# Optimization experiments

Measured on AMD Instinct MI355X. Metric: run time of the kernel, lower is better.

Reference implementation:

```python
import jax, jax.numpy as jnp
import numpy as np

EPS = 1e-5  # torch GroupNorm default eps

def gn(x, g, b):
    # GroupNorm with 1 group on [..., C]: normalize over channel dim, per-channel affine
    m = jnp.mean(x, axis=-1, keepdims=True)
    v = jnp.var(x, axis=-1, keepdims=True)
    return (x - m) * jax.lax.rsqrt(v + EPS) * g + b

def linear_res(x, W1, g1, b1, W2, g2, b2):
    # LaneGCN LinearRes (n_in == n_out, identity shortcut)
    out = jax.nn.relu(gn(x @ W1, g1, b1))
    out = gn(out @ W2, g2, b2)
    return jax.nn.relu(out + x)

def setup_inputs() -> dict:
    key = jax.random.key(0)
    N, K, P, D = 100000, 6, 30, 128
    ks = jax.random.split(key, 12)
    s = 0.05
    f32 = jnp.float32
    return dict(
        actors=jax.random.normal(ks[0], (N, D), f32),
        actor_ctrs=jax.random.normal(ks[1], (N, 2), f32) * 50.0,
        pred_W1=jax.random.normal(ks[2], (K, D, D), f32) * s,
        pred_g1=jnp.ones((K, D), f32), pred_b1=jnp.zeros((K, D), f32),
        pred_W2=jax.random.normal(ks[3], (K, D, D), f32) * s,
        pred_g2=jnp.ones((K, D), f32), pred_b2=jnp.zeros((K, D), f32),
        pred_Wo=jax.random.normal(ks[4], (K, D, 2 * P), f32) * s,
        pred_bo=jnp.zeros((K, 2 * P), f32),
        dist_W0=jax.random.normal(ks[5], (2, D), f32) * s,
        dist_b0=jnp.zeros((D,), f32),
        dist_W1=jax.random.normal(ks[6], (D, D), f32) * s,
        dist_g1=jnp.ones((D,), f32), dist_b1=jnp.zeros((D,), f32),
        agt_W=jax.random.normal(ks[7], (2 * D, D), f32) * s,
        agt_g=jnp.ones((D,), f32), agt_b=jnp.zeros((D,), f32),
        cls_W1=jax.random.normal(ks[8], (D, D), f32) * s,
        cls_g1=jnp.ones((D,), f32), cls_b1=jnp.zeros((D,), f32),
        cls_W2=jax.random.normal(ks[9], (D, D), f32) * s,
        cls_g2=jnp.ones((D,), f32), cls_b2=jnp.zeros((D,), f32),
        cls_Wo=jax.random.normal(ks[10], (D, 1), f32) * s,
        cls_bo=jnp.zeros((1,), f32),
    )

def reference(actors, actor_ctrs,
              pred_W1, pred_g1, pred_b1, pred_W2, pred_g2, pred_b2, pred_Wo, pred_bo,
              dist_W0, dist_b0, dist_W1, dist_g1, dist_b1,
              agt_W, agt_g, agt_b,
              cls_W1, cls_g1, cls_b1, cls_W2, cls_g2, cls_b2, cls_Wo, cls_bo):
    N, D = actors.shape
    K = pred_W1.shape[0]
    # --- num_mods prediction heads (LinearRes + Linear), vectorized over K ---
    h = jnp.einsum('nd,kde->kne', actors, pred_W1)
    h = jax.nn.relu(gn(h, pred_g1[:, None, :], pred_b1[:, None, :]))
    h = gn(jnp.einsum('kne,kef->knf', h, pred_W2), pred_g2[:, None, :], pred_b2[:, None, :])
    h = jax.nn.relu(h + actors[None])
    preds = jnp.einsum('knd,kdo->kno', h, pred_Wo) + pred_bo[:, None, :]   # [K,N,2P]
    reg = jnp.transpose(preds, (1, 0, 2)).reshape(N, K, -1, 2)             # [N,K,P,2]
    reg = reg + actor_ctrs[:, None, None, :]
    dest_ctrs = jax.lax.stop_gradient(reg[:, :, -1, :])                     # [N,K,2] (detach)
    # --- destination attention (myAttDestNoMap), vectorized over K modes ---
    dist = actor_ctrs[:, None, :] - dest_ctrs                              # [N,K,2]
    dh = jax.nn.relu(dist @ dist_W0 + dist_b0)
    dh = jax.nn.relu(gn(dh @ dist_W1, dist_g1, dist_b1))
    cat = jnp.concatenate([dh, jnp.broadcast_to(actors[:, None, :], (N, K, D))], axis=-1)
    feats = jax.nn.relu(gn(cat @ agt_W, agt_g, agt_b)).reshape(N * K, D)   # [N*K, D]
    # --- classification head + mode sorting ---
    c = linear_res(feats, cls_W1, cls_g1, cls_b1, cls_W2, cls_g2, cls_b2)
    cls = (c @ cls_Wo + cls_bo).reshape(N, K)
    cls = jax.nn.softmax(cls, axis=1)
    sort_idcs = jnp.argsort(-cls, axis=1)
    cls_sorted = jnp.take_along_axis(cls, sort_idcs, axis=1)               # [N,K]
    reg_sorted = jnp.take_along_axis(reg, sort_idcs[:, :, None, None], axis=1)  # [N,K,P,2]
    return cls_sorted, reg_sorted, feats
```

## Files before the change

kernel.cpp:

```cpp
#include <hip/hip_runtime.h>

#define NTOT 100000
#define KMOD 6

typedef short bf16x8 __attribute__((ext_vector_type(8)));
typedef float f32x4  __attribute__((ext_vector_type(4)));
typedef unsigned short u16x8 __attribute__((ext_vector_type(8)));

#define G1   0
#define B1O  128
#define G2   256
#define B2O  384
#define W0A  512
#define W0B  640
#define B0O  768
#define DG1  896
#define DB1  1024
#define AGTG 1152
#define AGTB 1280
#define CG1  1408
#define CB1O 1536
#define CG2  1664
#define CB2O 1792
#define CWO  1920
#define PBO  2048

__device__ __forceinline__ unsigned short f2bf(float f){
  union { float f; unsigned u; } c; c.f = f;
  return (unsigned short)((c.u + 0x7FFFu + ((c.u >> 16) & 1u)) >> 16);
}
__device__ __forceinline__ float bf2f(unsigned short h){
  union { unsigned u; float f; } c; c.u = ((unsigned)h) << 16; return c.f;
}

__global__ void prep_w(const float* __restrict__ W1, const float* __restrict__ W2,
                       const float* __restrict__ Wo, const float* __restrict__ dW1,
                       const float* __restrict__ agW, const float* __restrict__ cW1,
                       const float* __restrict__ cW2, unsigned short* __restrict__ dst){
  int e = blockIdx.x * 256 + threadIdx.x;
  if (e >= 327680) return;
  const float* base; int m = 0, r, CB = 8, Dreal = 128, mstride = 16384;
  if (e < 98304)       { base = W1;  m = e / 16384; r = e % 16384; }
  else if (e < 196608) { int x = e - 98304;  base = W2; m = x / 16384; r = x % 16384; }
  else if (e < 245760) { int x = e - 196608; base = Wo; m = x / 8192;  r = x % 8192; CB = 4; Dreal = 60; mstride = 7680; }
  else if (e < 262144) { base = dW1; r = e - 245760; }
  else if (e < 294912) { base = agW; r = e - 262144; }
  else if (e < 311296) { base = cW1; r = e - 294912; }
  else                 { base = cW2; r = e - 311296; }
  int per = CB * 512;
  int ks = r / per, rr = r % per;
  int cb = rr >> 9, l = (rr >> 3) & 63, j = rr & 7;
  int d = ks * 32 + ((l >> 4) << 3) + j;
  int c = (cb << 4) + (l & 15);
  float v = (c < Dreal) ? base[(size_t)m * mstride + d * Dreal + c] : 0.f;
  dst[e] = f2bf(v);
}

template<int CBN>
__device__ __forceinline__ void gemm2(const char* __restrict__ wsrc,
                                      const unsigned short* __restrict__ Xin,
                                      unsigned short* __restrict__ Wc, f32x4* acc){
  const int t = threadIdx.x, lane = t & 63, w = t >> 6;
  constexpr int chunk_bytes = CBN * 2048;
  constexpr int iters = chunk_bytes / 16 / 256;
  #pragma unroll
  for (int c = 0; c < 2; ++c){
    __syncthreads();
    const uint4* src = (const uint4*)(wsrc + c * chunk_bytes);
    uint4* dstv = (uint4*)Wc;
    #pragma unroll
    for (int i = 0; i < iters; ++i) dstv[t + i * 256] = src[t + i * 256];
    __syncthreads();
    #pragma unroll
    for (int ksl = 0; ksl < 2; ++ksl){
      const int ks = c * 2 + ksl;
      bf16x8 a = *(const bf16x8*)(Xin + ((w * 4 + ks) * 64 + lane) * 8);
      const unsigned short* wb = Wc + (ksl * CBN * 64 + lane) * 8;
      #pragma unroll
      for (int cb = 0; cb < CBN; ++cb){
        bf16x8 b = *(const bf16x8*)(wb + cb * 512);
        acc[cb] = __builtin_amdgcn_mfma_f32_16x16x32_bf16(a, b, acc[cb], 0, 0, 0);
      }
    }
  }
}

__device__ __forceinline__ void row_stats8(const f32x4* acc, float* mean, float* rstd){
  #pragma unroll
  for (int i = 0; i < 4; ++i){
    float s = 0.f, qq = 0.f;
    #pragma unroll
    for (int cb = 0; cb < 8; ++cb){ float v = acc[cb][i]; s += v; qq += v * v; }
    #pragma unroll
    for (int m = 1; m < 16; m <<= 1){ s += __shfl_xor(s, m, 16); qq += __shfl_xor(qq, m, 16); }
    float mu = s * 0.0078125f;
    float var = qq * 0.0078125f - mu * mu;
    mean[i] = mu; rstd[i] = rsqrtf(var + 1e-5f);
  }
}

__device__ __forceinline__ void epi_gn(const f32x4* acc, const float* cst, int goff, int boff,
                                       const unsigned short* res, unsigned short* Xout,
                                       float* feats_out, int n0, int kk){
  const int t = threadIdx.x, lane = t & 63, w = t >> 6, q = lane >> 4, c0 = lane & 15;
  float mean[4], rstd[4];
  row_stats8(acc, mean, rstd);
  #pragma unroll
  for (int cb = 0; cb < 8; ++cb){
    int col = c0 + (cb << 4);
    float g = cst[goff + col], bb = cst[boff + col];
    int base = ((w * 4 + (col >> 5)) * 64 + ((col >> 3) & 3) * 16) * 8 + (col & 7);
    #pragma unroll
    for (int i = 0; i < 4; ++i){
      int r15 = (q << 2) + i;
      float v = (acc[cb][i] - mean[i]) * rstd[i] * g + bb;
      if (res) v += bf2f(res[base + r15 * 8]);
      v = fmaxf(v, 0.f);
      if (feats_out){
        int n = n0 + w * 16 + r15;
        if (n < NTOT) feats_out[(size_t)(n * KMOD + kk) * 128 + col] = v;
      }
      Xout[base + r15 * 8] = f2bf(v);
    }
  }
}

#define ZACC(a, n) { _Pragma("unroll") for (int z = 0; z < (n); ++z){ (a)[z][0]=0.f;(a)[z][1]=0.f;(a)[z][2]=0.f;(a)[z][3]=0.f; } }

__global__ __launch_bounds__(256, 2) void meg(
    const float* __restrict__ actors, const float* __restrict__ ctrs,
    const float* __restrict__ pg1, const float* __restrict__ pb1,
    const float* __restrict__ pg2, const float* __restrict__ pb2,
    const float* __restrict__ pbo, const float* __restrict__ dW0, const float* __restrict__ db0,
    const float* __restrict__ dg1, const float* __restrict__ db1v,
    const float* __restrict__ agg, const float* __restrict__ agb,
    const float* __restrict__ cg1v, const float* __restrict__ cb1v,
    const float* __restrict__ cg2v, const float* __restrict__ cb2v,
    const float* __restrict__ cWo, const float* __restrict__ cbo,
    const unsigned short* __restrict__ wprep, float* __restrict__ logits,
    float* __restrict__ out_reg, float* __restrict__ out_feats){

  __shared__ __align__(16) unsigned short A0[8192];
  __shared__ __align__(16) unsigned short X1[8192];
  __shared__ __align__(16) unsigned short X2[8192];
  __shared__ __align__(16) unsigned short Wc[8192];
  __shared__ float cst[2176];
  __shared__ float ctr_l[128];
  __shared__ float dist_l[128];

  const int t = threadIdx.x;
  const int kk = blockIdx.x % KMOD;
  const int tile = blockIdx.x / KMOD;
  const int n0 = tile * 64;
  const int valid = min(64, NTOT - n0);
  const float cbo_v = cbo[0];

  if (t < 128){
    cst[G1 + t]   = pg1[kk * 128 + t];
    cst[B1O + t]  = pb1[kk * 128 + t];
    cst[G2 + t]   = pg2[kk * 128 + t];
    cst[B2O + t]  = pb2[kk * 128 + t];
    cst[W0A + t]  = dW0[t];
    cst[W0B + t]  = dW0[128 + t];
    cst[B0O + t]  = db0[t];
    cst[DG1 + t]  = dg1[t];
    cst[DB1 + t]  = db1v[t];
    cst[AGTG + t] = agg[t];
    cst[AGTB + t] = agb[t];
    cst[CG1 + t]  = cg1v[t];
    cst[CB1O + t] = cb1v[t];
    cst[CG2 + t]  = cg2v[t];
    cst[CB2O + t] = cb2v[t];
    cst[CWO + t]  = cWo[t];
  } else if (t < 192){
    int i = t - 128;
    cst[PBO + i] = (i < 60) ? pbo[kk * 60 + i] : 0.f;
  } else {
    int row = t - 192;
    if (row < valid){
      ctr_l[row * 2]     = ctrs[(size_t)(n0 + row) * 2];
      ctr_l[row * 2 + 1] = ctrs[(size_t)(n0 + row) * 2 + 1];
    } else { ctr_l[row * 2] = 0.f; ctr_l[row * 2 + 1] = 0.f; }
  }

  #pragma unroll
  for (int ii = 0; ii < 8; ++ii){
    int e2 = t + ii * 256;
    int row = e2 >> 5, c4 = e2 & 31;
    float4 v = make_float4(0.f, 0.f, 0.f, 0.f);
    if (row < valid) v = *(const float4*)(actors + (size_t)(n0 + row) * 128 + c4 * 4);
    int colb = c4 * 4;
    int idx = (((row >> 4) * 4 + (colb >> 5)) * 64 + (row & 15) + (((colb >> 3) & 3) << 4)) * 8 + (colb & 7);
    A0[idx]     = f2bf(v.x); A0[idx + 1] = f2bf(v.y);
    A0[idx + 2] = f2bf(v.z); A0[idx + 3] = f2bf(v.w);
  }

  const char* wp = (const char*)wprep;
  const char* W1k  = wp + (size_t)kk * 32768;
  const char* W2k  = wp + 196608 + (size_t)kk * 32768;
  const char* Wok  = wp + 393216 + (size_t)kk * 16384;
  const char* dW1p = wp + 491520;
  const char* agtp = wp + 524288;
  const char* cW1p = wp + 589824;
  const char* cW2p = wp + 622592;

  const int lane = t & 63, w = t >> 6, q = lane >> 4, c0 = lane & 15;
  f32x4 acc[8];

  ZACC(acc, 8);
  gemm2<8>(W1k, A0, Wc, acc);
  epi_gn(acc, cst, G1, B1O, nullptr, X1, nullptr, n0, kk);

  ZACC(acc, 8);
  gemm2<8>(W2k, X1, Wc, acc);
  epi_gn(acc, cst, G2, B2O, A0, X2, nullptr, n0, kk);

  {
    f32x4 acc4[4]; ZACC(acc4, 4);
    gemm2<4>(Wok, X2, Wc, acc4);
    #pragma unroll
    for (int cb = 0; cb < 4; ++cb){
      int col = c0 + (cb << 4);
      float bo = cst[PBO + col];
      #pragma unroll
      for (int i = 0; i < 4; ++i){
        int row = w * 16 + (q << 2) + i;
        float v = acc4[cb][i] + bo;
        if (col == 58) dist_l[row * 2]     = -v;
        if (col == 59) dist_l[row * 2 + 1] = -v;
        int n = n0 + row;
        if (col < 60 && n < NTOT)
          out_reg[(size_t)(n * KMOD + kk) * 60 + col] = v + ctr_l[row * 2 + (col & 1)];
      }
    }
  }
  __syncthreads();

  {
    int r15 = lane & 15;
    int row = w * 16 + r15;
    float d0 = dist_l[row * 2], d1 = dist_l[row * 2 + 1];
    #pragma unroll
    for (int ks = 0; ks < 4; ++ks){
      int dbase = ks * 32 + ((lane >> 4) << 3);
      u16x8 pack;
      #pragma unroll
      for (int j = 0; j < 8; ++j){
        int d = dbase + j;
        float v = fmaxf(d0 * cst[W0A + d] + d1 * cst[W0B + d] + cst[B0O + d], 0.f);
        pack[j] = f2bf(v);
      }
      *(u16x8*)(X1 + ((w * 4 + ks) * 64 + lane) * 8) = pack;
    }
  }

  ZACC(acc, 8);
  gemm2<8>(dW1p, X1, Wc, acc);
  epi_gn(acc, cst, DG1, DB1, nullptr, X2, nullptr, n0, kk);

  ZACC(acc, 8);
  gemm2<8>(agtp, X2, Wc, acc);
  gemm2<8>(agtp + 32768, A0, Wc, acc);
  epi_gn(acc, cst, AGTG, AGTB, nullptr, X1, out_feats, n0, kk);

  ZACC(acc, 8);
  gemm2<8>(cW1p, X1, Wc, acc);
  epi_gn(acc, cst, CG1, CB1O, nullptr, X2, nullptr, n0, kk);

  ZACC(acc, 8);
  gemm2<8>(cW2p, X2, Wc, acc);
  {
    float mean[4], rstd[4];
    row_stats8(acc, mean, rstd);
    float part[4] = {0.f, 0.f, 0.f, 0.f};
    #pragma unroll
    for (int cb = 0; cb < 8; ++cb){
      int col = c0 + (cb << 4);
      float g = cst[CG2 + col], bb = cst[CB2O + col], wo = cst[CWO + col];
      int base = ((w * 4 + (col >> 5)) * 64 + ((col >> 3) & 3) * 16) * 8 + (col & 7);
      #pragma unroll
      for (int i = 0; i < 4; ++i){
        int r15 = (q << 2) + i;
        float v = (acc[cb][i] - mean[i]) * rstd[i] * g + bb;
        v += bf2f(X1[base + r15 * 8]);
        v = fmaxf(v, 0.f);
        part[i] += v * wo;
      }
    }
    #pragma unroll
    for (int i = 0; i < 4; ++i){
      #pragma unroll
      for (int m = 1; m < 16; m <<= 1) part[i] += __shfl_xor(part[i], m, 16);
    }
    if (c0 == 0){
      #pragma unroll
      for (int i = 0; i < 4; ++i){
        int n = n0 + w * 16 + (q << 2) + i;
        if (n < NTOT) logits[n * KMOD + kk] = part[i] + cbo_v;
      }
    }
  }
}

__global__ __launch_bounds__(256) void fin(const float* __restrict__ logits,
                                           float* __restrict__ out_cls,
                                           float* __restrict__ out_reg){
  const int wid = blockIdx.x * 4 + (threadIdx.x >> 6);
  const int lane = threadIdx.x & 63;
  if (wid >= NTOT) return;
  const int n = wid;
  float lg[6];
  #pragma unroll
  for (int k2 = 0; k2 < 6; ++k2) lg[k2] = logits[n * 6 + k2];
  float mx = lg[0];
  #pragma unroll
  for (int k2 = 1; k2 < 6; ++k2) mx = fmaxf(mx, lg[k2]);
  float ex[6]; float s = 0.f;
  #pragma unroll
  for (int k2 = 0; k2 < 6; ++k2){ ex[k2] = expf(lg[k2] - mx); s += ex[k2]; }
  float inv = 1.f / s;
  int rank[6];
  #pragma unroll
  for (int k2 = 0; k2 < 6; ++k2){
    int r = 0;
    #pragma unroll
    for (int j2 = 0; j2 < 6; ++j2) r += (lg[j2] > lg[k2]) || (lg[j2] == lg[k2] && j2 < k2);
    rank[k2] = r;
  }
  if (lane < 6){
    float pv = 0.f;
    #pragma unroll
    for (int k2 = 0; k2 < 6; ++k2) pv += (rank[k2] == lane) ? ex[k2] : 0.f;
    out_cls[n * 6 + lane] = pv * inv;
  }
  if (lane < 60){
    float v[6];
    #pragma unroll
    for (int k2 = 0; k2 < 6; ++k2) v[k2] = out_reg[(size_t)(n * 6 + k2) * 60 + lane];
    #pragma unroll
    for (int r2 = 0; r2 < 6; ++r2){
      float ov = 0.f;
      #pragma unroll
      for (int k2 = 0; k2 < 6; ++k2) ov += (rank[k2] == r2) ? v[k2] : 0.f;
      out_reg[(size_t)(n * 6 + r2) * 60 + lane] = ov;
    }
  }
}

extern "C" void kernel_launch(void* const* d_in, const int* in_sizes, int n_in,
                              void* d_out, int out_size, void* d_ws, size_t ws_size,
                              hipStream_t stream){
  const float* actors = (const float*)d_in[0];
  const float* ctrs   = (const float*)d_in[1];
  const float* pW1 = (const float*)d_in[2];
  const float* pg1 = (const float*)d_in[3];
  const float* pb1 = (const float*)d_in[4];
  const float* pW2 = (const float*)d_in[5];
  const float* pg2 = (const float*)d_in[6];
  const float* pb2 = (const float*)d_in[7];
  const float* pWo = (const float*)d_in[8];
  const float* pbo = (const float*)d_in[9];
  const float* dW0 = (const float*)d_in[10];
  const float* db0 = (const float*)d_in[11];
  const float* dW1 = (const float*)d_in[12];
  const float* dg1 = (const float*)d_in[13];
  const float* db1 = (const float*)d_in[14];
  const float* agW = (const float*)d_in[15];
  const float* agg = (const float*)d_in[16];
  const float* agb = (const float*)d_in[17];
  const float* cW1 = (const float*)d_in[18];
  const float* cg1 = (const float*)d_in[19];
  const float* cb1 = (const float*)d_in[20];
  const float* cW2 = (const float*)d_in[21];
  const float* cg2 = (const float*)d_in[22];
  const float* cb2 = (const float*)d_in[23];
  const float* cWo = (const float*)d_in[24];
  const float* cbo = (const float*)d_in[25];

  float* logits = (float*)d_ws;
  unsigned short* wprep = (unsigned short*)((char*)d_ws + 2400256);
  float* out = (float*)d_out;
  float* out_cls   = out;
  float* out_reg   = out + 600000;
  float* out_feats = out + 36600000;

  hipLaunchKernelGGL(prep_w, dim3(1280), dim3(256), 0, stream,
                     pW1, pW2, pWo, dW1, agW, cW1, cW2, wprep);
  hipLaunchKernelGGL(meg, dim3(((NTOT + 63) / 64) * KMOD), dim3(256), 0, stream,
                     actors, ctrs, pg1, pb1, pg2, pb2, pbo, dW0, db0, dg1, db1,
                     agg, agb, cg1, cb1, cg2, cb2, cWo, cbo, wprep, logits, out_reg, out_feats);
  hipLaunchKernelGGL(fin, dim3(NTOT / 4), dim3(256), 0, stream, logits, out_cls, out_reg);
}
```

Before: 1.068 ms.

## Double-buffer weight loads via global_load_lds and use nontemporal output stores

Replaces the synchronous register-staged copy of weight chunks into LDS with direct global-to-LDS loads, issued per k-step into two alternating buffers so the next slice loads while MFMAs run on the current one. Large output writes (feats, regression) become nontemporal stores so they do not pollute cache. The manual waitcnt and barrier handling adds more barriers per GEMM (one before and one after each k-step) and is fragile if the vmcnt counts are wrong.

Result: faster. 1.041 ms (-2.5%).

```diff
diff --git a/kernel.cpp b/kernel.cpp
--- a/kernel.cpp
+++ b/kernel.cpp
@@ -31,6 +31,12 @@
 }
 __device__ __forceinline__ float bf2f(unsigned short h){
   union { unsigned u; float f; } c; c.u = ((unsigned)h) << 16; return c.f;
+}
+
+__device__ __forceinline__ void gload16(const void* g, void* l){
+  __builtin_amdgcn_global_load_lds(
+      (const __attribute__((address_space(1))) unsigned int*)g,
+      (__attribute__((address_space(3))) unsigned int*)l, 16, 0, 0);
 }
 
 __global__ void prep_w(const float* __restrict__ W1, const float* __restrict__ W2,
@@ -61,27 +67,40 @@
                                       const unsigned short* __restrict__ Xin,
                                       unsigned short* __restrict__ Wc, f32x4* acc){
   const int t = threadIdx.x, lane = t & 63, w = t >> 6;
-  constexpr int chunk_bytes = CBN * 2048;
-  constexpr int iters = chunk_bytes / 16 / 256;
-  #pragma unroll
-  for (int c = 0; c < 2; ++c){
-    __syncthreads();
-    const uint4* src = (const uint4*)(wsrc + c * chunk_bytes);
-    uint4* dstv = (uint4*)Wc;
-    #pragma unroll
-    for (int i = 0; i < iters; ++i) dstv[t + i * 256] = src[t + i * 256];
-    __syncthreads();
-    #pragma unroll
-    for (int ksl = 0; ksl < 2; ++ksl){
-      const int ks = c * 2 + ksl;
-      bf16x8 a = *(const bf16x8*)(Xin + ((w * 4 + ks) * 64 + lane) * 8);
-      const unsigned short* wb = Wc + (ksl * CBN * 64 + lane) * 8;
-      #pragma unroll
-      for (int cb = 0; cb < CBN; ++cb){
-        bf16x8 b = *(const bf16x8*)(wb + cb * 512);
-        acc[cb] = __builtin_amdgcn_mfma_f32_16x16x32_bf16(a, b, acc[cb], 0, 0, 0);
-      }
-    }
+  constexpr int kbytes = CBN * 1024;
+  constexpr int nld = kbytes / 4096;
+  char* wlds = (char*)Wc;
+  asm volatile("s_waitcnt lgkmcnt(0)" ::: "memory");
+  __builtin_amdgcn_s_barrier();
+  asm volatile("" ::: "memory");
+  #pragma unroll
+  for (int i = 0; i < nld; ++i)
+    gload16(wsrc + (t + i * 256) * 16, wlds + (t + i * 256) * 16);
+  #pragma unroll
+  for (int k = 0; k < 4; ++k){
+    if (k < 3){
+      const char* src = wsrc + (k + 1) * kbytes;
+      char* dstp = wlds + ((k + 1) & 1) * kbytes;
+      #pragma unroll
+      for (int i = 0; i < nld; ++i)
+        gload16(src + (t + i * 256) * 16, dstp + (t + i * 256) * 16);
+      if constexpr (nld == 2) asm volatile("s_waitcnt vmcnt(2)" ::: "memory");
+      else                    asm volatile("s_waitcnt vmcnt(1)" ::: "memory");
+    } else {
+      asm volatile("s_waitcnt vmcnt(0)" ::: "memory");
+    }
+    __builtin_amdgcn_s_barrier();
+    asm volatile("" ::: "memory");
+    bf16x8 a = *(const bf16x8*)(Xin + ((w * 4 + k) * 64 + lane) * 8);
+    const unsigned short* wb = Wc + (k & 1) * CBN * 512 + lane * 8;
+    #pragma unroll
+    for (int cb = 0; cb < CBN; ++cb){
+      bf16x8 b = *(const bf16x8*)(wb + cb * 512);
+      acc[cb] = __builtin_amdgcn_mfma_f32_16x16x32_bf16(a, b, acc[cb], 0, 0, 0);
+    }
+    asm volatile("s_waitcnt lgkmcnt(0)" ::: "memory");
+    __builtin_amdgcn_s_barrier();
+    asm volatile("" ::: "memory");
   }
 }
 
@@ -118,7 +137,8 @@
       v = fmaxf(v, 0.f);
       if (feats_out){
         int n = n0 + w * 16 + r15;
-        if (n < NTOT) feats_out[(size_t)(n * KMOD + kk) * 128 + col] = v;
+        if (n < NTOT)
+          __builtin_nontemporal_store(v, &feats_out[(size_t)(n * KMOD + kk) * 128 + col]);
       }
       Xout[base + r15 * 8] = f2bf(v);
     }
@@ -230,7 +250,8 @@
         if (col == 59) dist_l[row * 2 + 1] = -v;
         int n = n0 + row;
         if (col < 60 && n < NTOT)
-          out_reg[(size_t)(n * KMOD + kk) * 60 + col] = v + ctr_l[row * 2 + (col & 1)];
+          __builtin_nontemporal_store(v + ctr_l[row * 2 + (col & 1)],
+                                      &out_reg[(size_t)(n * KMOD + kk) * 60 + col]);
       }
     }
   }
```

## Stream GEMM weights from global into registers, removing LDS staging and block barriers

Applied to the files above, without the earlier changes.

Weights are no longer cooperatively copied into a shared Wc buffer between __syncthreads. Each wave now reads its B fragments directly from global or L2 into registers with double buffering, and the A fragments are held in registers. Per-layer constants are read straight from global instead of being staged in shared memory. Activation loading is remapped so each wave writes only its own rows, which lets the block barrier be replaced with a wave-local waitcnt. This cuts LDS footprint and block-level syncs, which should raise occupancy, but each wave now fetches the full weight matrix itself, so global and L2 traffic goes up several-fold.

Result: faster. 985.1 us (-7.7%).

```diff
diff --git a/kernel.cpp b/kernel.cpp
--- a/kernel.cpp
+++ b/kernel.cpp
@@ -6,24 +6,7 @@
 typedef short bf16x8 __attribute__((ext_vector_type(8)));
 typedef float f32x4  __attribute__((ext_vector_type(4)));
 typedef unsigned short u16x8 __attribute__((ext_vector_type(8)));
-
-#define G1   0
-#define B1O  128
-#define G2   256
-#define B2O  384
-#define W0A  512
-#define W0B  640
-#define B0O  768
-#define DG1  896
-#define DB1  1024
-#define AGTG 1152
-#define AGTB 1280
-#define CG1  1408
-#define CB1O 1536
-#define CG2  1664
-#define CB2O 1792
-#define CWO  1920
-#define PBO  2048
+typedef unsigned short u16x4 __attribute__((ext_vector_type(4)));
 
 __device__ __forceinline__ unsigned short f2bf(float f){
   union { float f; unsigned u; } c; c.f = f;
@@ -57,30 +40,30 @@
 }
 
 template<int CBN>
-__device__ __forceinline__ void gemm2(const char* __restrict__ wsrc,
-                                      const unsigned short* __restrict__ Xin,
-                                      unsigned short* __restrict__ Wc, f32x4* acc){
+__device__ __forceinline__ void gemmR(const char* __restrict__ wsrc,
+                                      const unsigned short* __restrict__ Xin, f32x4* acc){
   const int t = threadIdx.x, lane = t & 63, w = t >> 6;
-  constexpr int chunk_bytes = CBN * 2048;
-  constexpr int iters = chunk_bytes / 16 / 256;
-  #pragma unroll
-  for (int c = 0; c < 2; ++c){
-    __syncthreads();
-    const uint4* src = (const uint4*)(wsrc + c * chunk_bytes);
-    uint4* dstv = (uint4*)Wc;
-    #pragma unroll
-    for (int i = 0; i < iters; ++i) dstv[t + i * 256] = src[t + i * 256];
-    __syncthreads();
-    #pragma unroll
-    for (int ksl = 0; ksl < 2; ++ksl){
-      const int ks = c * 2 + ksl;
-      bf16x8 a = *(const bf16x8*)(Xin + ((w * 4 + ks) * 64 + lane) * 8);
-      const unsigned short* wb = Wc + (ksl * CBN * 64 + lane) * 8;
-      #pragma unroll
-      for (int cb = 0; cb < CBN; ++cb){
-        bf16x8 b = *(const bf16x8*)(wb + cb * 512);
-        acc[cb] = __builtin_amdgcn_mfma_f32_16x16x32_bf16(a, b, acc[cb], 0, 0, 0);
-      }
+  bf16x8 a[4];
+  #pragma unroll
+  for (int ks = 0; ks < 4; ++ks)
+    a[ks] = *(const bf16x8*)(Xin + ((w * 4 + ks) * 64 + lane) * 8);
+  const char* wl = wsrc + lane * 16;
+  bf16x8 bb[2][4];
+  #pragma unroll
+  for (int i = 0; i < 4; ++i)
+    bb[0][i] = *(const bf16x8*)(wl + i * 1024);
+  #pragma unroll
+  for (int g = 0; g < CBN; ++g){
+    if (g + 1 < CBN){
+      #pragma unroll
+      for (int i = 0; i < 4; ++i)
+        bb[(g + 1) & 1][i] = *(const bf16x8*)(wl + ((g + 1) * 4 + i) * 1024);
+    }
+    #pragma unroll
+    for (int i = 0; i < 4; ++i){
+      const int fi = g * 4 + i;
+      acc[fi % CBN] = __builtin_amdgcn_mfma_f32_16x16x32_bf16(
+          a[fi / CBN], bb[g & 1][i], acc[fi % CBN], 0, 0, 0);
     }
   }
 }
@@ -99,7 +82,8 @@
   }
 }
 
-__device__ __forceinline__ void epi_gn(const f32x4* acc, const float* cst, int goff, int boff,
+__device__ __forceinline__ void epi_gn(const f32x4* acc, const float* __restrict__ gptr,
+                                       const float* __restrict__ bptr,
                                        const unsigned short* res, unsigned short* Xout,
                                        float* feats_out, int n0, int kk){
   const int t = threadIdx.x, lane = t & 63, w = t >> 6, q = lane >> 4, c0 = lane & 15;
@@ -108,7 +92,7 @@
   #pragma unroll
   for (int cb = 0; cb < 8; ++cb){
     int col = c0 + (cb << 4);
-    float g = cst[goff + col], bb = cst[boff + col];
+    float g = gptr[col], bb = bptr[col];
     int base = ((w * 4 + (col >> 5)) * 64 + ((col >> 3) & 3) * 16) * 8 + (col & 7);
     #pragma unroll
     for (int i = 0; i < 4; ++i){
@@ -143,56 +127,36 @@
   __shared__ __align__(16) unsigned short A0[8192];
   __shared__ __align__(16) unsigned short X1[8192];
   __shared__ __align__(16) unsigned short X2[8192];
-  __shared__ __align__(16) unsigned short Wc[8192];
-  __shared__ float cst[2176];
   __shared__ float ctr_l[128];
   __shared__ float dist_l[128];
 
-  const int t = threadIdx.x;
+  const int t = threadIdx.x, lane = t & 63, w = t >> 6;
   const int kk = blockIdx.x % KMOD;
   const int tile = blockIdx.x / KMOD;
   const int n0 = tile * 64;
   const int valid = min(64, NTOT - n0);
   const float cbo_v = cbo[0];
 
-  if (t < 128){
-    cst[G1 + t]   = pg1[kk * 128 + t];
-    cst[B1O + t]  = pb1[kk * 128 + t];
-    cst[G2 + t]   = pg2[kk * 128 + t];
-    cst[B2O + t]  = pb2[kk * 128 + t];
-    cst[W0A + t]  = dW0[t];
-    cst[W0B + t]  = dW0[128 + t];
-    cst[B0O + t]  = db0[t];
-    cst[DG1 + t]  = dg1[t];
-    cst[DB1 + t]  = db1v[t];
-    cst[AGTG + t] = agg[t];
-    cst[AGTB + t] = agb[t];
-    cst[CG1 + t]  = cg1v[t];
-    cst[CB1O + t] = cb1v[t];
-    cst[CG2 + t]  = cg2v[t];
-    cst[CB2O + t] = cb2v[t];
-    cst[CWO + t]  = cWo[t];
-  } else if (t < 192){
-    int i = t - 128;
-    cst[PBO + i] = (i < 60) ? pbo[kk * 60 + i] : 0.f;
-  } else {
-    int row = t - 192;
-    if (row < valid){
-      ctr_l[row * 2]     = ctrs[(size_t)(n0 + row) * 2];
-      ctr_l[row * 2 + 1] = ctrs[(size_t)(n0 + row) * 2 + 1];
-    } else { ctr_l[row * 2] = 0.f; ctr_l[row * 2 + 1] = 0.f; }
-  }
-
-  #pragma unroll
-  for (int ii = 0; ii < 8; ++ii){
-    int e2 = t + ii * 256;
-    int row = e2 >> 5, c4 = e2 & 31;
-    float4 v = make_float4(0.f, 0.f, 0.f, 0.f);
-    if (row < valid) v = *(const float4*)(actors + (size_t)(n0 + row) * 128 + c4 * 4);
-    int colb = c4 * 4;
-    int idx = (((row >> 4) * 4 + (colb >> 5)) * 64 + (row & 15) + (((colb >> 3) & 3) << 4)) * 8 + (colb & 7);
-    A0[idx]     = f2bf(v.x); A0[idx + 1] = f2bf(v.y);
-    A0[idx + 2] = f2bf(v.z); A0[idx + 3] = f2bf(v.w);
+  if (lane < 32){
+    int r = lane >> 1, which = lane & 1;
+    int row = w * 16 + r;
+    ctr_l[row * 2 + which] = (row < valid) ? ctrs[(size_t)(n0 + row) * 2 + which] : 0.f;
+  }
+
+  {
+    int r15 = lane >> 2, cq = lane & 3;
+    int row = w * 16 + r15;
+    const float* arow = actors + (size_t)(n0 + row) * 128;
+    #pragma unroll
+    for (int ii = 0; ii < 8; ++ii){
+      int c4 = cq * 8 + ii;
+      float4 v = make_float4(0.f, 0.f, 0.f, 0.f);
+      if (row < valid) v = *(const float4*)(arow + c4 * 4);
+      int colb = c4 * 4;
+      int idx = ((w * 4 + (colb >> 5)) * 64 + r15 + (((colb >> 3) & 3) << 4)) * 8 + (colb & 7);
+      u16x4 p; p[0] = f2bf(v.x); p[1] = f2bf(v.y); p[2] = f2bf(v.z); p[3] = f2bf(v.w);
+      *(u16x4*)(A0 + idx) = p;
+    }
   }
 
   const char* wp = (const char*)wprep;
@@ -204,24 +168,24 @@
   const char* cW1p = wp + 589824;
   const char* cW2p = wp + 622592;
 
-  const int lane = t & 63, w = t >> 6, q = lane >> 4, c0 = lane & 15;
+  const int q = lane >> 4, c0 = lane & 15;
   f32x4 acc[8];
 
   ZACC(acc, 8);
-  gemm2<8>(W1k, A0, Wc, acc);
-  epi_gn(acc, cst, G1, B1O, nullptr, X1, nullptr, n0, kk);
-
-  ZACC(acc, 8);
-  gemm2<8>(W2k, X1, Wc, acc);
-  epi_gn(acc, cst, G2, B2O, A0, X2, nullptr, n0, kk);
+  gemmR<8>(W1k, A0, acc);
+  epi_gn(acc, pg1 + kk * 128, pb1 + kk * 128, nullptr, X1, nullptr, n0, kk);
+
+  ZACC(acc, 8);
+  gemmR<8>(W2k, X1, acc);
+  epi_gn(acc, pg2 + kk * 128, pb2 + kk * 128, A0, X2, nullptr, n0, kk);
 
   {
     f32x4 acc4[4]; ZACC(acc4, 4);
-    gemm2<4>(Wok, X2, Wc, acc4);
+    gemmR<4>(Wok, X2, acc4);
     #pragma unroll
     for (int cb = 0; cb < 4; ++cb){
       int col = c0 + (cb << 4);
-      float bo = cst[PBO + col];
+      float bo = (col < 60) ? pbo[kk * 60 + col] : 0.f;
       #pragma unroll
       for (int i = 0; i < 4; ++i){
         int row = w * 16 + (q << 2) + i;
@@ -234,7 +198,8 @@
       }
     }
   }
-  __syncthreads();
+  asm volatile("s_waitcnt lgkmcnt(0)" ::: "memory");
+  __builtin_amdgcn_sched_barrier(0);
 
   {
     int r15 = lane & 15;
@@ -243,32 +208,40 @@
     #pragma unroll
     for (int ks = 0; ks < 4; ++ks){
       int dbase = ks * 32 + ((lane >> 4) << 3);
+      float4 wa0 = *(const float4*)(dW0 + dbase);
+      float4 wa1 = *(const float4*)(dW0 + dbase + 4);
+      float4 wb0 = *(const float4*)(dW0 + 128 + dbase);
+      float4 wb1 = *(const float4*)(dW0 + 128 + dbase + 4);
+      float4 b00 = *(const float4*)(db0 + dbase);
+      float4 b01 = *(const float4*)(db0 + dbase + 4);
       u16x8 pack;
-      #pragma unroll
-      for (int j = 0; j < 8; ++j){
-        int d = dbase + j;
-        float v = fmaxf(d0 * cst[W0A + d] + d1 * cst[W0B + d] + cst[B0O + d], 0.f);
-        pack[j] = f2bf(v);
-      }
+      pack[0] = f2bf(fmaxf(d0 * wa0.x + d1 * wb0.x + b00.x, 0.f));
+      pack[1] = f2bf(fmaxf(d0 * wa0.y + d1 * wb0.y + b00.y, 0.f));
+      pack[2] = f2bf(fmaxf(d0 * wa0.z + d1 * wb0.z + b00.z, 0.f));
+      pack[3] = f2bf(fmaxf(d0 * wa0.w + d1 * wb0.w + b00.w, 0.f));
+      pack[4] = f2bf(fmaxf(d0 * wa1.x + d1 * wb1.x + b01.x, 0.f));
+      pack[5] = f2bf(fmaxf(d0 * wa1.y + d1 * wb1.y + b01.y, 0.f));
+      pack[6] = f2bf(fmaxf(d0 * wa1.z + d1 * wb1.z + b01.z, 0.f));
+      pack[7] = f2bf(fmaxf(d0 * wa1.w + d1 * wb1.w + b01.w, 0.f));
       *(u16x8*)(X1 + ((w * 4 + ks) * 64 + lane) * 8) = pack;
     }
   }
 
   ZACC(acc, 8);
-  gemm2<8>(dW1p, X1, Wc, acc);
-  epi_gn(acc, cst, DG1, DB1, nullptr, X2, nullptr, n0, kk);
-
-  ZACC(acc, 8);
-  gemm2<8>(agtp, X2, Wc, acc);
-  gemm2<8>(agtp + 32768, A0, Wc, acc);
-  epi_gn(acc, cst, AGTG, AGTB, nullptr, X1, out_feats, n0, kk);
-
-  ZACC(acc, 8);
-  gemm2<8>(cW1p, X1, Wc, acc);
-  epi_gn(acc, cst, CG1, CB1O, nullptr, X2, nullptr, n0, kk);
-
-  ZACC(acc, 8);
-  gemm2<8>(cW2p, X2, Wc, acc);
+  gemmR<8>(dW1p, X1, acc);
+  epi_gn(acc, dg1, db1v, nullptr, X2, nullptr, n0, kk);
+
+  ZACC(acc, 8);
+  gemmR<8>(agtp, X2, acc);
+  gemmR<8>(agtp + 32768, A0, acc);
+  epi_gn(acc, agg, agb, nullptr, X1, out_feats, n0, kk);
+
+  ZACC(acc, 8);
+  gemmR<8>(cW1p, X1, acc);
+  epi_gn(acc, cg1v, cb1v, nullptr, X2, nullptr, n0, kk);
+
+  ZACC(acc, 8);
+  gemmR<8>(cW2p, X2, acc);
   {
     float mean[4], rstd[4];
     row_stats8(acc, mean, rstd);
@@ -276,7 +249,7 @@
     #pragma unroll
     for (int cb = 0; cb < 8; ++cb){
       int col = c0 + (cb << 4);
-      float g = cst[CG2 + col], bb = cst[CB2O + col], wo = cst[CWO + col];
+      float g = cg2v[col], bb = cb2v[col], wo = cWo[col];
       int base = ((w * 4 + (col >> 5)) * 64 + ((col >> 3) & 3) * 16) * 8 + (col & 7);
       #pragma unroll
       for (int i = 0; i < 4; ++i){
```
